# Optimization experiments

Measured on AMD Instinct MI355X. Metric: run time of the kernel, lower is better.

## Reference

```python
import jax, jax.numpy as jnp
import numpy as np

D_MODEL = 1024
NUM_HEADS = 16
HEAD_DIM = D_MODEL // NUM_HEADS
B, S, L_CACHE = 2, 1024, 1024


def setup_inputs() -> dict:
    key = jax.random.key(0)
    ks = jax.random.split(key, 12)
    sc = 1.0 / np.sqrt(D_MODEL)
    return {
        "x": jax.random.normal(ks[0], (B, S, D_MODEL), jnp.float32),
        "cache_k": jax.random.normal(ks[1], (B, NUM_HEADS, L_CACHE, HEAD_DIM), jnp.float32),
        "cache_v": jax.random.normal(ks[2], (B, NUM_HEADS, L_CACHE, HEAD_DIM), jnp.float32),
        "Wq": jax.random.normal(ks[3], (D_MODEL, D_MODEL), jnp.float32) * sc,
        "bq": jax.random.normal(ks[4], (D_MODEL,), jnp.float32) * 0.01,
        "Wk": jax.random.normal(ks[5], (D_MODEL, D_MODEL), jnp.float32) * sc,
        "bk": jax.random.normal(ks[6], (D_MODEL,), jnp.float32) * 0.01,
        "Wv": jax.random.normal(ks[7], (D_MODEL, D_MODEL), jnp.float32) * sc,
        "bv": jax.random.normal(ks[8], (D_MODEL,), jnp.float32) * 0.01,
        "Wo": jax.random.normal(ks[9], (D_MODEL, D_MODEL), jnp.float32) * sc,
        "bo": jax.random.normal(ks[10], (D_MODEL,), jnp.float32) * 0.01,
    }


def reference(x, cache_k, cache_v, Wq, bq, Wk, bk, Wv, bv, Wo, bo):
    b, s, d = x.shape
    h, hd = NUM_HEADS, HEAD_DIM
    # torch Linear: y = x @ W^T + b
    def proj(W, bias):
        y = jnp.einsum('bsd,ed->bse', x, W) + bias
        return y.reshape(b, s, h, hd).transpose(0, 2, 1, 3)  # [B,H,S,hd]
    Q = proj(Wq, bq)
    K = jnp.concatenate([cache_k, proj(Wk, bk)], axis=2)  # [B,H,T,hd]
    V = jnp.concatenate([cache_v, proj(Wv, bv)], axis=2)
    T = K.shape[2]
    scores = jnp.einsum('bhqd,bhkd->bhqk', Q, K) / jnp.sqrt(jnp.float32(hd))
    # causal mask with cache offset: query i sees keys j <= i + (T - s)
    offset = T - s
    q_idx = jnp.arange(s)[:, None]
    k_idx = jnp.arange(T)[None, :]
    mask = k_idx > (q_idx + offset)  # [S,T], True = masked
    scores = jnp.where(mask[None, None], -jnp.inf, scores)
    attn = jax.nn.softmax(scores, axis=-1)
    out = jnp.einsum('bhqk,bhkd->bhqd', attn, V)
    out = out.transpose(0, 2, 1, 3).reshape(b, s, d)
    return jnp.einsum('bsd,ed->bse', out, Wo) + bo
```

## Files before the change

### kernel.cpp

```cpp
#include <hip/hip_runtime.h>
#include <hip/hip_bf16.h>
#include <stdint.h>

typedef __bf16 bf16;
typedef __bf16 bf16x4 __attribute__((ext_vector_type(4)));
typedef __bf16 bf16x8 __attribute__((ext_vector_type(8)));
typedef float  f32x4  __attribute__((ext_vector_type(4)));

#define DEV __device__ __forceinline__

#define BB 2
#define HH 16
#define SS 1024
#define DD 1024
#define HD 64
#define LC 1024
#define TT 2048
#define OFFS 1024

DEV f32x4 mfma16(bf16x8 a, bf16x8 b, f32x4 c) {
    return __builtin_amdgcn_mfma_f32_16x16x32_bf16(a, b, c, 0, 0, 0);
}

DEV void async_load16(const bf16* g, bf16* lds) {
    auto gp = reinterpret_cast<const __attribute__((address_space(1))) void*>(
        reinterpret_cast<uintptr_t>(g));
    auto lp = reinterpret_cast<__attribute__((address_space(3))) void*>(
        reinterpret_cast<uintptr_t>(lds));
    __builtin_amdgcn_global_load_lds(gp, lp, 16, 0, 0);
}

DEV bf16x8 cvt8(float4 a, float4 b) {
    bf16x8 o;
    o[0] = (bf16)a.x; o[1] = (bf16)a.y; o[2] = (bf16)a.z; o[3] = (bf16)a.w;
    o[4] = (bf16)b.x; o[5] = (bf16)b.y; o[6] = (bf16)b.z; o[7] = (bf16)b.w;
    return o;
}

__global__ __launch_bounds__(256) void cvt_all(
    const float* __restrict__ x,  bf16* __restrict__ xb,
    const float* __restrict__ w0, const float* __restrict__ w1,
    const float* __restrict__ w2, const float* __restrict__ w3,
    bf16* __restrict__ d0, bf16* __restrict__ d1,
    bf16* __restrict__ d2, bf16* __restrict__ d3,
    const float* __restrict__ ck, bf16* __restrict__ Kf,
    const float* __restrict__ cv, bf16* __restrict__ Vt) {
    __shared__ float tile[64][65];
    const int bid = blockIdx.x;
    const int tid = threadIdx.x;
    if (bid < 4096) {
        const float* s;
        bf16* d;
        int i;
        if (bid < 1024) {
            s = x; d = xb; i = bid * 512 + tid * 2;
        } else if (bid < 3072) {
            int which = (bid - 1024) >> 9;
            s = which == 0 ? w0 : which == 1 ? w1 : which == 2 ? w2 : w3;
            d = which == 0 ? d0 : which == 1 ? d1 : which == 2 ? d2 : d3;
            i = ((bid - 1024) & 511) * 512 + tid * 2;
        } else {
            int ii = (bid - 3072) * 512 + tid * 2;
            int bh  = ii >> 14;
            int rem = ii & 16383;
            float4 a = ((const float4*)ck)[ii];
            float4 b = ((const float4*)ck)[ii + 1];
            ((bf16x8*)(Kf + (size_t)bh * TT * HD))[rem >> 1] = cvt8(a, b);
            return;
        }
        float4 a = ((const float4*)s)[i];
        float4 b = ((const float4*)s)[i + 1];
        ((bf16x8*)d)[i >> 1] = cvt8(a, b);
    } else {
        int rem = bid - 4096;
        int bh = rem >> 4;
        int t0 = (rem & 15) * 64;
        int c4 = (tid & 15) * 4;
        int rr = tid >> 4;
        const float* src = cv + ((size_t)bh * LC + t0) * HD;
#pragma unroll
        for (int p = 0; p < 4; ++p) {
            int t = rr + p * 16;
            float4 v = *(const float4*)(src + (size_t)t * HD + c4);
            tile[c4 + 0][t] = v.x; tile[c4 + 1][t] = v.y;
            tile[c4 + 2][t] = v.z; tile[c4 + 3][t] = v.w;
        }
        __syncthreads();
        bf16* dst = Vt + (size_t)bh * HD * TT + t0;
#pragma unroll
        for (int p = 0; p < 4; ++p) {
            int d = rr + p * 16;
            int tc = (tid & 15) * 4;
            bf16x4 o;
            o[0] = (bf16)tile[d][tc + 0]; o[1] = (bf16)tile[d][tc + 1];
            o[2] = (bf16)tile[d][tc + 2]; o[3] = (bf16)tile[d][tc + 3];
            *(bf16x4*)(dst + (size_t)d * TT + tc) = o;
        }
    }
}

__global__ __launch_bounds__(256) void gemm_nt(
    const bf16* __restrict__ A, const bf16* __restrict__ W,
    const float* __restrict__ bq, const float* __restrict__ bk,
    const float* __restrict__ bv,
    bf16* __restrict__ Qb, bf16* __restrict__ Kf, bf16* __restrict__ Vt) {
    const int tid  = threadIdx.x;
    const int wv   = tid >> 6;
    const int lane = tid & 63;
    const int l16  = lane & 15;
    const int quad = lane >> 4;
    const int m0 = blockIdx.y * 64;
    const int n0 = blockIdx.x * 128;
    const int mode = n0 >> 10;
    const float* bias = (mode == 0) ? bq : (mode == 1) ? bk : bv;

    __shared__ __align__(16) bf16 As[2][64 * 64];
    __shared__ __align__(16) bf16 Bs[2][128 * 64];

    f32x4 acc[4][2];
#pragma unroll
    for (int i = 0; i < 4; ++i)
#pragma unroll
        for (int j = 0; j < 2; ++j) {
            f32x4 z = {0.f, 0.f, 0.f, 0.f};
            acc[i][j] = z;
        }

    auto stage = [&](int k0, int b) {
#pragma unroll
        for (int k = 0; k < 2; ++k) {
            int seg = k * 256 + tid;
            int row = seg >> 3;
            int c   = (seg & 7) ^ (row & 7);
            async_load16(A + (size_t)(m0 + row) * 1024 + k0 + c * 8, &As[b][seg * 8]);
        }
#pragma unroll
        for (int k = 0; k < 4; ++k) {
            int seg = k * 256 + tid;
            int row = seg >> 3;
            int c   = (seg & 7) ^ (row & 7);
            async_load16(W + (size_t)(n0 + row) * 1024 + k0 + c * 8, &Bs[b][seg * 8]);
        }
    };

    stage(0, 0);

    for (int it = 0; it < 16; ++it) {
        __syncthreads();
        const bf16* Ab = &As[it & 1][0];
        const bf16* Bb = &Bs[it & 1][0];
        if (it + 1 < 16) stage((it + 1) * 64, (it + 1) & 1);

#pragma unroll
        for (int kk = 0; kk < 2; ++kk) {
            bf16x8 af[4], bfr[2];
#pragma unroll
            for (int i = 0; i < 4; ++i) {
                int row = i * 16 + l16;
                int slot = (kk * 4 + quad) ^ (row & 7);
                af[i] = *(const bf16x8*)(Ab + (row * 8 + slot) * 8);
            }
#pragma unroll
            for (int j = 0; j < 2; ++j) {
                int row = wv * 32 + j * 16 + l16;
                int slot = (kk * 4 + quad) ^ (row & 7);
                bfr[j] = *(const bf16x8*)(Bb + (row * 8 + slot) * 8);
            }
#pragma unroll
            for (int i = 0; i < 4; ++i)
#pragma unroll
                for (int j = 0; j < 2; ++j)
                    acc[i][j] = mfma16(af[i], bfr[j], acc[i][j]);
        }
    }

#pragma unroll
    for (int i = 0; i < 4; ++i) {
#pragma unroll
        for (int j = 0; j < 2; ++j) {
            int n = n0 + wv * 32 + j * 16 + l16;
            float bval = bias[n & 1023];
#pragma unroll
            for (int r = 0; r < 4; ++r) {
                int m = m0 + i * 16 + quad * 4 + r;
                float v = acc[i][j][r] + bval;
                int b = m >> 10, s = m & 1023;
                int h = (n & 1023) >> 6, d = n & 63;
                int bh = b * HH + h;
                if (mode == 0)
                    Qb[((size_t)bh * SS + s) * HD + d] = (bf16)v;
                else if (mode == 1)
                    Kf[((size_t)bh * TT + LC + s) * HD + d] = (bf16)v;
                else
                    Vt[((size_t)bh * HD + d) * TT + LC + s] = (bf16)v;
            }
        }
    }
}

__global__ __launch_bounds__(256) void gemm_oproj(
    const bf16* __restrict__ A, const bf16* __restrict__ W,
    const float* __restrict__ bo, float* __restrict__ Out) {
    const int tid  = threadIdx.x;
    const int wv   = tid >> 6;
    const int lane = tid & 63;
    const int l16  = lane & 15;
    const int quad = lane >> 4;
    const int m0 = blockIdx.y * 32;
    const int n0 = blockIdx.x * 128;

    __shared__ __align__(16) bf16 As[2][32 * 64];
    __shared__ __align__(16) bf16 Bs[2][128 * 64];

    f32x4 acc[2][2];
#pragma unroll
    for (int i = 0; i < 2; ++i)
#pragma unroll
        for (int j = 0; j < 2; ++j) {
            f32x4 z = {0.f, 0.f, 0.f, 0.f};
            acc[i][j] = z;
        }

    auto stage = [&](int k0, int b) {
        {
            int seg = tid;
            int row = seg >> 3;
            int c   = (seg & 7) ^ (row & 7);
            async_load16(A + (size_t)(m0 + row) * 1024 + k0 + c * 8, &As[b][seg * 8]);
        }
#pragma unroll
        for (int k = 0; k < 4; ++k) {
            int seg = k * 256 + tid;
            int row = seg >> 3;
            int c   = (seg & 7) ^ (row & 7);
            async_load16(W + (size_t)(n0 + row) * 1024 + k0 + c * 8, &Bs[b][seg * 8]);
        }
    };

    stage(0, 0);

    for (int it = 0; it < 16; ++it) {
        __syncthreads();
        const bf16* Ab = &As[it & 1][0];
        const bf16* Bb = &Bs[it & 1][0];
        if (it + 1 < 16) stage((it + 1) * 64, (it + 1) & 1);

#pragma unroll
        for (int kk = 0; kk < 2; ++kk) {
            bf16x8 af[2], bfr[2];
#pragma unroll
            for (int i = 0; i < 2; ++i) {
                int row = i * 16 + l16;
                int slot = (kk * 4 + quad) ^ (row & 7);
                af[i] = *(const bf16x8*)(Ab + (row * 8 + slot) * 8);
            }
#pragma unroll
            for (int j = 0; j < 2; ++j) {
                int row = wv * 32 + j * 16 + l16;
                int slot = (kk * 4 + quad) ^ (row & 7);
                bfr[j] = *(const bf16x8*)(Bb + (row * 8 + slot) * 8);
            }
#pragma unroll
            for (int i = 0; i < 2; ++i)
#pragma unroll
                for (int j = 0; j < 2; ++j)
                    acc[i][j] = mfma16(af[i], bfr[j], acc[i][j]);
        }
    }

#pragma unroll
    for (int i = 0; i < 2; ++i) {
#pragma unroll
        for (int j = 0; j < 2; ++j) {
            int n = n0 + wv * 32 + j * 16 + l16;
            float bval = bo[n];
#pragma unroll
            for (int r = 0; r < 4; ++r) {
                int m = m0 + i * 16 + quad * 4 + r;
                Out[(size_t)m * 1024 + n] = acc[i][j][r] + bval;
            }
        }
    }
}

__global__ __launch_bounds__(256) void attn(const bf16* __restrict__ Qb,
                                            const bf16* __restrict__ Kf,
                                            const bf16* __restrict__ Vt,
                                            bf16* __restrict__ Ob) {
    const int i = blockIdx.x;
    const int bh = i & 31;
    const int qblk = 15 - (i >> 5);
    const int tid  = threadIdx.x;
    const int wv   = tid >> 6;
    const int qh   = wv & 1;
    const int kh   = wv >> 1;
    const int lane = tid & 63;
    const int l16  = lane & 15;
    const int quad = lane >> 4;
    const int qb   = qblk * 64;
    const int qw   = qb + qh * 32;
    const int kbase = kh * 64;

    const bf16* Qp = Qb + ((size_t)bh * SS + qw) * HD;
    const bf16* Kp = Kf + (size_t)bh * TT * HD;
    const bf16* Vp = Vt + (size_t)bh * HD * TT;

    __shared__ __align__(16) bf16 Ks[2][128 * 64];
    __shared__ __align__(16) bf16 Vs[2][64 * 128];

    bf16x8 qf[2][2];
#pragma unroll
    for (int qs = 0; qs < 2; ++qs)
#pragma unroll
        for (int dc = 0; dc < 2; ++dc)
            qf[qs][dc] = *(const bf16x8*)(Qp + (qs * 16 + l16) * HD + dc * 32 + quad * 8);

    float lsum[2] = {0.f, 0.f};
    f32x4 o[4][2];
#pragma unroll
    for (int dt = 0; dt < 4; ++dt)
#pragma unroll
        for (int qs = 0; qs < 2; ++qs) {
            f32x4 z = {0.f, 0.f, 0.f, 0.f};
            o[dt][qs] = z;
        }

    const int niters = qblk / 2 + 9;

    auto stage = [&](int tile, int b) {
        const int t0 = tile * 128;
#pragma unroll
        for (int j = 0; j < 4; ++j) {
            int seg = j * 256 + tid;
            int krow = seg >> 3;
            int kc   = (seg & 7) ^ (krow & 7);
            async_load16(Kp + (size_t)(t0 + krow) * HD + kc * 8, &Ks[b][seg * 8]);
            int drow = seg >> 4;
            int tc   = (seg & 15) ^ (drow & 15);
            async_load16(Vp + (size_t)drow * TT + t0 + tc * 8, &Vs[b][seg * 8]);
        }
    };

    stage(0, 0);

    const float C1 = 0.18033688f;
    const float C2 = -11.5415603f;

    for (int it = 0; it < niters; ++it) {
        __syncthreads();
        const bf16* Kb = &Ks[it & 1][0];
        const bf16* Vb = &Vs[it & 1][0];
        if (it + 1 < niters) stage(it + 1, (it + 1) & 1);

        const int t0 = it * 128;
        if (t0 + kbase > qw + 31 + OFFS) continue;
        const bool full = (t0 + kbase + 63 <= qw + OFFS);

        f32x4 s[4][2];
#pragma unroll
        for (int kt = 0; kt < 4; ++kt) {
            int row = kbase + kt * 16 + l16;
            int swz = row & 7;
            bf16x8 ka = *(const bf16x8*)(Kb + (row * 8 + (quad ^ swz)) * 8);
            bf16x8 kb = *(const bf16x8*)(Kb + (row * 8 + ((4 + quad) ^ swz)) * 8);
#pragma unroll
            for (int qs = 0; qs < 2; ++qs) {
                f32x4 z = {0.f, 0.f, 0.f, 0.f};
                z = mfma16(ka, qf[qs][0], z);
                z = mfma16(kb, qf[qs][1], z);
                s[kt][qs] = z;
            }
        }

        f32x4 p[4][2];
        if (full) {
#pragma unroll
            for (int kt = 0; kt < 4; ++kt)
#pragma unroll
                for (int qs = 0; qs < 2; ++qs)
#pragma unroll
                    for (int r = 0; r < 4; ++r)
                        p[kt][qs][r] = __builtin_amdgcn_exp2f(fmaf(s[kt][qs][r], C1, C2));
        } else {
#pragma unroll
            for (int qs = 0; qs < 2; ++qs) {
                const int qlim = qw + qs * 16 + l16 + OFFS - t0;
#pragma unroll
                for (int kt = 0; kt < 4; ++kt)
#pragma unroll
                    for (int r = 0; r < 4; ++r) {
                        int tl = kbase + kt * 16 + quad * 4 + r;
                        float e = __builtin_amdgcn_exp2f(fmaf(s[kt][qs][r], C1, C2));
                        p[kt][qs][r] = (tl <= qlim) ? e : 0.f;
                    }
            }
        }
#pragma unroll
        for (int qs = 0; qs < 2; ++qs)
#pragma unroll
            for (int kt = 0; kt < 4; ++kt)
                lsum[qs] += (p[kt][qs][0] + p[kt][qs][1]) + (p[kt][qs][2] + p[kt][qs][3]);

        bf16x8 pf[2][2];
#pragma unroll
        for (int kf = 0; kf < 2; ++kf)
#pragma unroll
            for (int qs = 0; qs < 2; ++qs)
#pragma unroll
                for (int j = 0; j < 4; ++j) {
                    pf[kf][qs][j]     = (bf16)p[kf * 2][qs][j];
                    pf[kf][qs][4 + j] = (bf16)p[kf * 2 + 1][qs][j];
                }

        const int q1 = quad >> 1;
        const int h4 = (quad & 1) * 4;
#pragma unroll
        for (int dt = 0; dt < 4; ++dt) {
            int row = dt * 16 + l16;
            int swz = row & 15;
#pragma unroll
            for (int kf = 0; kf < 2; ++kf) {
                int c0 = kh * 8 + kf * 4 + q1;
                bf16x4 v0 = *(const bf16x4*)(Vb + (row * 16 + (c0 ^ swz)) * 8 + h4);
                bf16x4 v1 = *(const bf16x4*)(Vb + (row * 16 + ((c0 + 2) ^ swz)) * 8 + h4);
                bf16x8 vf;
#pragma unroll
                for (int j = 0; j < 4; ++j) {
                    vf[j] = v0[j]; vf[4 + j] = v1[j];
                }
#pragma unroll
                for (int qs = 0; qs < 2; ++qs)
                    o[dt][qs] = mfma16(vf, pf[kf][qs], o[dt][qs]);
            }
        }
    }

#pragma unroll
    for (int qs = 0; qs < 2; ++qs) {
        lsum[qs] += __shfl_xor(lsum[qs], 16, 64);
        lsum[qs] += __shfl_xor(lsum[qs], 32, 64);
    }

    __syncthreads();
    float* So = (float*)&Ks[0][0];
    float* Sl = (float*)&Vs[0][0];
    if (kh == 1) {
#pragma unroll
        for (int dt = 0; dt < 4; ++dt)
#pragma unroll
            for (int qs = 0; qs < 2; ++qs)
#pragma unroll
                for (int r = 0; r < 4; ++r)
                    So[(dt * 8 + qs * 4 + r) * 128 + qh * 64 + lane] = o[dt][qs][r];
#pragma unroll
        for (int qs = 0; qs < 2; ++qs)
            Sl[qs * 128 + qh * 64 + lane] = lsum[qs];
    }
    __syncthreads();
    if (kh == 1) return;

#pragma unroll
    for (int dt = 0; dt < 4; ++dt)
#pragma unroll
        for (int qs = 0; qs < 2; ++qs)
#pragma unroll
            for (int r = 0; r < 4; ++r)
                o[dt][qs][r] += So[(dt * 8 + qs * 4 + r) * 128 + qh * 64 + lane];
    float rl[2];
#pragma unroll
    for (int qs = 0; qs < 2; ++qs)
        rl[qs] = 1.f / (lsum[qs] + Sl[qs * 128 + qh * 64 + lane]);

    const int b = bh >> 4, h = bh & 15;
#pragma unroll
    for (int qs = 0; qs < 2; ++qs) {
        const int q = qw + qs * 16 + l16;
        bf16* op = Ob + (((size_t)(b * SS + q) * HH) + h) * HD;
#pragma unroll
        for (int dt = 0; dt < 4; ++dt) {
            bf16x4 w;
#pragma unroll
            for (int r = 0; r < 4; ++r) w[r] = (bf16)(o[dt][qs][r] * rl[qs]);
            *(bf16x4*)(op + dt * 16 + quad * 4) = w;
        }
    }
}

extern "C" void kernel_launch(void* const* d_in, const int* in_sizes, int n_in,
                              void* d_out, int out_size, void* d_ws, size_t ws_size,
                              hipStream_t stream) {
    const float* x   = (const float*)d_in[0];
    const float* ck  = (const float*)d_in[1];
    const float* cv  = (const float*)d_in[2];
    const float* Wq  = (const float*)d_in[3];
    const float* bq  = (const float*)d_in[4];
    const float* Wk  = (const float*)d_in[5];
    const float* bk  = (const float*)d_in[6];
    const float* Wv  = (const float*)d_in[7];
    const float* bv  = (const float*)d_in[8];
    const float* Wo  = (const float*)d_in[9];
    const float* bo  = (const float*)d_in[10];
    float* out = (float*)d_out;

    char* ws = (char*)d_ws;
    bf16* xb  = (bf16*)(ws);
    bf16* wqb = (bf16*)(ws + ( 4u << 20));
    bf16* wkb = (bf16*)(ws + ( 6u << 20));
    bf16* wvb = (bf16*)(ws + ( 8u << 20));
    bf16* wob = (bf16*)(ws + (10u << 20));
    bf16* Qb  = (bf16*)(ws + (12u << 20));
    bf16* Kf  = (bf16*)(ws + (16u << 20));
    bf16* Vt  = (bf16*)(ws + (24u << 20));
    bf16* Ob  = (bf16*)(ws + (32u << 20));

    cvt_all<<<4608, 256, 0, stream>>>(x, xb, Wq, Wk, Wv, Wo, wqb, wkb, wvb, wob,
                                      ck, Kf, cv, Vt);

    gemm_nt<<<dim3(24, 32), 256, 0, stream>>>(xb, wqb, bq, bk, bv, Qb, Kf, Vt);
    attn<<<512, 256, 0, stream>>>(Qb, Kf, Vt, Ob);
    gemm_oproj<<<dim3(8, 64), 256, 0, stream>>>(Ob, wob, bo, out);
}
```

Before: 157.9 us.

## Move KV-cache conversion into QKV GEMM launch to overlap with matmul

The cache K/V fp32-to-bf16 conversion and V transpose are moved out of the first conversion kernel into extra blocks of the QKV projection GEMM launch, with a flattened 1D grid and shared LDS buffer. The aim is to let memory-bound conversion blocks run alongside compute-bound GEMM tiles instead of serially before them. The GEMM kernel now reserves 48KB of LDS for every block, including the conversion ones, which may limit occupancy for those blocks.

```diff
diff --git a/kernel.cpp b/kernel.cpp
--- a/kernel.cpp
+++ b/kernel.cpp
@@ -37,85 +37,88 @@
     return o;
 }
 
-__global__ __launch_bounds__(256) void cvt_all(
+__global__ __launch_bounds__(256) void cvt_xw(
     const float* __restrict__ x,  bf16* __restrict__ xb,
     const float* __restrict__ w0, const float* __restrict__ w1,
     const float* __restrict__ w2, const float* __restrict__ w3,
     bf16* __restrict__ d0, bf16* __restrict__ d1,
-    bf16* __restrict__ d2, bf16* __restrict__ d3,
-    const float* __restrict__ ck, bf16* __restrict__ Kf,
-    const float* __restrict__ cv, bf16* __restrict__ Vt) {
-    __shared__ float tile[64][65];
+    bf16* __restrict__ d2, bf16* __restrict__ d3) {
     const int bid = blockIdx.x;
     const int tid = threadIdx.x;
-    if (bid < 4096) {
-        const float* s;
-        bf16* d;
-        int i;
-        if (bid < 1024) {
-            s = x; d = xb; i = bid * 512 + tid * 2;
-        } else if (bid < 3072) {
-            int which = (bid - 1024) >> 9;
-            s = which == 0 ? w0 : which == 1 ? w1 : which == 2 ? w2 : w3;
-            d = which == 0 ? d0 : which == 1 ? d1 : which == 2 ? d2 : d3;
-            i = ((bid - 1024) & 511) * 512 + tid * 2;
-        } else {
-            int ii = (bid - 3072) * 512 + tid * 2;
+    const float* s;
+    bf16* d;
+    int i;
+    if (bid < 1024) {
+        s = x; d = xb; i = bid * 512 + tid * 2;
+    } else {
+        int which = (bid - 1024) >> 9;
+        s = which == 0 ? w0 : which == 1 ? w1 : which == 2 ? w2 : w3;
+        d = which == 0 ? d0 : which == 1 ? d1 : which == 2 ? d2 : d3;
+        i = ((bid - 1024) & 511) * 512 + tid * 2;
+    }
+    float4 a = ((const float4*)s)[i];
+    float4 b = ((const float4*)s)[i + 1];
+    ((bf16x8*)d)[i >> 1] = cvt8(a, b);
+}
+
+__global__ __launch_bounds__(256) void gemm_qkv_cvt(
+    const bf16* __restrict__ A, const bf16* __restrict__ W,
+    const float* __restrict__ bq, const float* __restrict__ bk,
+    const float* __restrict__ bv,
+    bf16* __restrict__ Qb, bf16* __restrict__ Kf, bf16* __restrict__ Vt,
+    const float* __restrict__ ck, const float* __restrict__ cv) {
+    __shared__ __align__(16) char smem[49152];
+    const int bid = blockIdx.x;
+    const int tid = threadIdx.x;
+
+    if (bid >= 768) {
+        if (bid < 1792) {
+            int ii = (bid - 768) * 512 + tid * 2;
             int bh  = ii >> 14;
             int rem = ii & 16383;
             float4 a = ((const float4*)ck)[ii];
             float4 b = ((const float4*)ck)[ii + 1];
             ((bf16x8*)(Kf + (size_t)bh * TT * HD))[rem >> 1] = cvt8(a, b);
-            return;
-        }
-        float4 a = ((const float4*)s)[i];
-        float4 b = ((const float4*)s)[i + 1];
-        ((bf16x8*)d)[i >> 1] = cvt8(a, b);
-    } else {
-        int rem = bid - 4096;
-        int bh = rem >> 4;
-        int t0 = (rem & 15) * 64;
-        int c4 = (tid & 15) * 4;
-        int rr = tid >> 4;
-        const float* src = cv + ((size_t)bh * LC + t0) * HD;
-#pragma unroll
-        for (int p = 0; p < 4; ++p) {
-            int t = rr + p * 16;
-            float4 v = *(const float4*)(src + (size_t)t * HD + c4);
-            tile[c4 + 0][t] = v.x; tile[c4 + 1][t] = v.y;
-            tile[c4 + 2][t] = v.z; tile[c4 + 3][t] = v.w;
-        }
-        __syncthreads();
-        bf16* dst = Vt + (size_t)bh * HD * TT + t0;
-#pragma unroll
-        for (int p = 0; p < 4; ++p) {
-            int d = rr + p * 16;
-            int tc = (tid & 15) * 4;
-            bf16x4 o;
-            o[0] = (bf16)tile[d][tc + 0]; o[1] = (bf16)tile[d][tc + 1];
-            o[2] = (bf16)tile[d][tc + 2]; o[3] = (bf16)tile[d][tc + 3];
-            *(bf16x4*)(dst + (size_t)d * TT + tc) = o;
-        }
-    }
-}
-
-__global__ __launch_bounds__(256) void gemm_nt(
-    const bf16* __restrict__ A, const bf16* __restrict__ W,
-    const float* __restrict__ bq, const float* __restrict__ bk,
-    const float* __restrict__ bv,
-    bf16* __restrict__ Qb, bf16* __restrict__ Kf, bf16* __restrict__ Vt) {
-    const int tid  = threadIdx.x;
+        } else {
+            float (*tile)[65] = (float(*)[65])smem;
+            int rem = bid - 1792;
+            int bh = rem >> 4;
+            int t0 = (rem & 15) * 64;
+            int c4 = (tid & 15) * 4;
+            int rr = tid >> 4;
+            const float* src = cv + ((size_t)bh * LC + t0) * HD;
+#pragma unroll
+            for (int p = 0; p < 4; ++p) {
+                int t = rr + p * 16;
+                float4 v = *(const float4*)(src + (size_t)t * HD + c4);
+                tile[c4 + 0][t] = v.x; tile[c4 + 1][t] = v.y;
+                tile[c4 + 2][t] = v.z; tile[c4 + 3][t] = v.w;
+            }
+            __syncthreads();
+            bf16* dst = Vt + (size_t)bh * HD * TT + t0;
+#pragma unroll
+            for (int p = 0; p < 4; ++p) {
+                int d = rr + p * 16;
+                int tc = (tid & 15) * 4;
+                bf16x4 o;
+                o[0] = (bf16)tile[d][tc + 0]; o[1] = (bf16)tile[d][tc + 1];
+                o[2] = (bf16)tile[d][tc + 2]; o[3] = (bf16)tile[d][tc + 3];
+                *(bf16x4*)(dst + (size_t)d * TT + tc) = o;
+            }
+        }
+        return;
+    }
+
+    bf16* As = (bf16*)smem;
+    bf16* Bs = (bf16*)(smem + 16384);
     const int wv   = tid >> 6;
     const int lane = tid & 63;
     const int l16  = lane & 15;
     const int quad = lane >> 4;
-    const int m0 = blockIdx.y * 64;
-    const int n0 = blockIdx.x * 128;
+    const int m0 = (bid & 31) * 64;
+    const int n0 = (bid >> 5) * 128;
     const int mode = n0 >> 10;
     const float* bias = (mode == 0) ? bq : (mode == 1) ? bk : bv;
-
-    __shared__ __align__(16) bf16 As[2][64 * 64];
-    __shared__ __align__(16) bf16 Bs[2][128 * 64];
 
     f32x4 acc[4][2];
 #pragma unroll
@@ -132,14 +135,16 @@
             int seg = k * 256 + tid;
             int row = seg >> 3;
             int c   = (seg & 7) ^ (row & 7);
-            async_load16(A + (size_t)(m0 + row) * 1024 + k0 + c * 8, &As[b][seg * 8]);
+            async_load16(A + (size_t)(m0 + row) * 1024 + k0 + c * 8,
+                         As + b * 4096 + seg * 8);
         }
 #pragma unroll
         for (int k = 0; k < 4; ++k) {
             int seg = k * 256 + tid;
             int row = seg >> 3;
             int c   = (seg & 7) ^ (row & 7);
-            async_load16(W + (size_t)(n0 + row) * 1024 + k0 + c * 8, &Bs[b][seg * 8]);
+            async_load16(W + (size_t)(n0 + row) * 1024 + k0 + c * 8,
+                         Bs + b * 8192 + seg * 8);
         }
     };
 
@@ -147,8 +152,8 @@
 
     for (int it = 0; it < 16; ++it) {
         __syncthreads();
-        const bf16* Ab = &As[it & 1][0];
-        const bf16* Bb = &Bs[it & 1][0];
+        const bf16* Ab = As + (it & 1) * 4096;
+        const bf16* Bb = Bs + (it & 1) * 8192;
         if (it + 1 < 16) stage((it + 1) * 64, (it + 1) & 1);
 
 #pragma unroll
@@ -513,10 +518,11 @@
     bf16* Vt  = (bf16*)(ws + (24u << 20));
     bf16* Ob  = (bf16*)(ws + (32u << 20));
 
-    cvt_all<<<4608, 256, 0, stream>>>(x, xb, Wq, Wk, Wv, Wo, wqb, wkb, wvb, wob,
-                                      ck, Kf, cv, Vt);
-
-    gemm_nt<<<dim3(24, 32), 256, 0, stream>>>(xb, wqb, bq, bk, bv, Qb, Kf, Vt);
+    cvt_xw<<<3072, 256, 0, stream>>>(x, xb, Wq, Wk, Wv, Wo, wqb, wkb, wvb, wob);
+
+    gemm_qkv_cvt<<<2304, 256, 0, stream>>>(xb, wqb, bq, bk, bv, Qb, Kf, Vt, ck, cv);
+
     attn<<<512, 256, 0, stream>>>(Qb, Kf, Vt, Ob);
+
     gemm_oproj<<<dim3(8, 64), 256, 0, stream>>>(Ob, wob, bo, out);
 }
```

New measurement: 153.8 us. 2.6% less time.
